# Performance work log

Hardware: AMD Instinct MI355X
Metric: run time of the kernel (lower is better)

## Reference

```python
import jax, jax.numpy as jnp
import numpy as np

V, E, L, T, H, B = 8124, 1024, 24, 512, 16, 2
S = E // H
DFF = E * 8 // 3  # 2730
EPS = 1e-5
SCALE = 1.0 / np.sqrt(E)  # note: 1/sqrt(emb_dim), as in the source


def _pe():
    # sinusoidal positional encoding [T, E]
    pos = jnp.arange(T, dtype=jnp.float32)[:, None]
    div = jnp.exp(jnp.arange(0, E, 2, dtype=jnp.float32) * (-np.log(10000.0) / E))
    pe = jnp.zeros((T, E), jnp.float32)
    pe = pe.at[:, 0::2].set(jnp.sin(pos * div))
    pe = pe.at[:, 1::2].set(jnp.cos(pos * div))
    return pe


def _rms(x, g):
    # NOTE: source takes the mean over the WHOLE tensor (no dim arg)
    rms = jnp.sqrt(jnp.mean(x.astype(jnp.float32) ** 2) + EPS)
    return (x / rms * g).astype(x.dtype)


def setup_inputs() -> dict:
    key = jax.random.key(0)
    ks = jax.random.split(key, 9)
    def w(k, shape):
        return jax.random.normal(k, shape, jnp.float32) * 0.02
    return {
        "tokens": jax.random.randint(ks[0], (B, T), 0, V),
        "emb_table": w(ks[1], (V, E)),
        "Wqkv": w(ks[2], (L, E, 3 * E)), "bqkv": jnp.zeros((L, 3 * E), jnp.float32),
        "Wo": w(ks[3], (L, E, E)), "bo": jnp.zeros((L, E), jnp.float32),
        "W1": w(ks[4], (L, E, DFF)), "b1": jnp.zeros((L, DFF), jnp.float32),
        "W3": w(ks[5], (L, E, DFF)), "b3": jnp.zeros((L, DFF), jnp.float32),
        "W2": w(ks[6], (L, DFF, E)), "b2": jnp.zeros((L, E), jnp.float32),
        "g_mha": jnp.ones((L, E), jnp.float32),
        "g_ff": jnp.ones((L, E), jnp.float32),
        "g_final": jnp.ones((E,), jnp.float32),
        "Wout": w(ks[7], (E, V)), "bout": jnp.zeros((V,), jnp.float32),
    }


def reference(tokens, emb_table, Wqkv, bqkv, Wo, bo, W1, b1, W3, b3, W2, b2,
              g_mha, g_ff, g_final, Wout, bout):
    x = emb_table[tokens] + _pe()[None]  # [B,T,E]
    mask = jnp.tril(jnp.ones((T, T), bool))

    def block(x, p):
        wqkv, bq, wo, bo_, w1, b1_, w3, b3_, w2, b2_, gm, gf = p
        # --- causal MHA ---
        y = _rms(x, gm)
        qkv = (y @ wqkv + bq).reshape(B, T, H, 3, S)
        q = qkv[..., 0, :].transpose(0, 2, 1, 3)  # [B,H,T,S]
        k = qkv[..., 1, :].transpose(0, 2, 1, 3)
        v = qkv[..., 2, :].transpose(0, 2, 1, 3)
        attn = jnp.einsum('bhqd,bhkd->bhqk', q, k).astype(jnp.float32) * SCALE
        attn = jnp.where(mask, attn, -jnp.inf)
        attn = jax.nn.softmax(attn, axis=-1).astype(x.dtype)
        y = jnp.einsum('bhqk,bhkd->bhqd', attn, v)
        y = y.transpose(0, 2, 1, 3).reshape(B, T, E)
        x = x + (y @ wo + bo_)
        # --- SwiGLU FFN ---
        h = _rms(x, gf)
        u = h @ w1 + b1_
        u = u * jax.nn.sigmoid(u) * (h @ w3 + b3_)
        return x + (u @ w2 + b2_), None

    x, _ = jax.lax.scan(block, x, (Wqkv, bqkv, Wo, bo, W1, b1, W3, b3, W2, b2, g_mha, g_ff))
    return _rms(x, g_final) @ Wout + bout  # [B,T,V]
```

## Files before the change

kernel.cpp:

```cpp
#include <hip/hip_runtime.h>
#include <hip/hip_bf16.h>
#include <math.h>

#define EDIM   1024
#define TSEQ   512
#define NBATCH 2
#define NHEAD  16
#define HDIM   64
#define NLAYER 24
#define VOCAB  8124
#define DFFDIM 2730
#define DPAD   2752
#define MTOK   (NBATCH*TSEQ)
#define NELEM  (MTOK*EDIM)
#define EPSF   1e-5f
#define SCALEF (1.0f/32.0f)
#define NEGBIG (-1e30f)

typedef __bf16 bf16x8 __attribute__((ext_vector_type(8)));
typedef __bf16 bf16x4 __attribute__((ext_vector_type(4)));
typedef float  f32x4  __attribute__((ext_vector_type(4)));

#define MFMA(a, b, c) __builtin_amdgcn_mfma_f32_16x16x32_bf16((a), (b), (c), 0, 0, 0)

__device__ __forceinline__ void gl_lds16(const __bf16* g, __bf16* l) {
  __builtin_amdgcn_global_load_lds(
      (const __attribute__((address_space(1))) void*)g,
      (__attribute__((address_space(3))) void*)l, 16, 0, 0);
}
template <int N> __device__ __forceinline__ void vmwait() {
  asm volatile("s_waitcnt vmcnt(%0)" :: "n"(N) : "memory");
}
__device__ __forceinline__ void lgkm_barrier() {
  asm volatile("s_waitcnt lgkmcnt(0)" ::: "memory");
  __builtin_amdgcn_s_barrier();
}

__global__ __launch_bounds__(256) void k_embed(const int* __restrict__ tok,
                                               const float* __restrict__ emb,
                                               float* __restrict__ x) {
  const int bt = blockIdx.x;
  const int t  = bt & (TSEQ - 1);
  const int tk = tok[bt];
  const float* er = emb + (size_t)tk * EDIM;
  float* xr = x + (size_t)bt * EDIM;
  for (int e = threadIdx.x * 4; e < EDIM; e += 256 * 4) {
    float4 v = *(const float4*)(er + e);
    float vv[4] = {v.x, v.y, v.z, v.w};
    float ou[4];
#pragma unroll
    for (int j = 0; j < 4; ++j) {
      int ee = e + j;
      int i2 = ee & ~1;
      float freq = expf(-(float)i2 * (9.210340371976184f / 1024.0f));
      float ang  = (float)t * freq;
      ou[j] = vv[j] + ((ee & 1) ? cosf(ang) : sinf(ang));
    }
    *(float4*)(xr + e) = make_float4(ou[0], ou[1], ou[2], ou[3]);
  }
}

__global__ __launch_bounds__(256) void k_red1f(float* __restrict__ x,
                                               const float* __restrict__ pb,
                                               int np,
                                               const float* __restrict__ bias,
                                               float* __restrict__ part) {
  float s = 0.f;
  const bool fold = (pb != nullptr);
  for (int i = (blockIdx.x * 256 + threadIdx.x) * 4; i < NELEM; i += 256 * 256 * 4) {
    float4 v = *(const float4*)(x + i);
    if (fold) {
      for (int z = 0; z < np; ++z) {
        float4 a = *(const float4*)(pb + (size_t)z * NELEM + i);
        v.x += a.x; v.y += a.y; v.z += a.z; v.w += a.w;
      }
      float4 c = *(const float4*)(bias + (i & (EDIM - 1)));
      v.x += c.x; v.y += c.y; v.z += c.z; v.w += c.w;
      *(float4*)(x + i) = v;
    }
    s += v.x * v.x + v.y * v.y + v.z * v.z + v.w * v.w;
  }
#pragma unroll
  for (int o = 32; o > 0; o >>= 1) s += __shfl_down(s, o);
  __shared__ float sm[4];
  if ((threadIdx.x & 63) == 0) sm[threadIdx.x >> 6] = s;
  __syncthreads();
  if (threadIdx.x == 0) part[blockIdx.x] = sm[0] + sm[1] + sm[2] + sm[3];
}

__device__ __forceinline__ void conv_tile(const float* __restrict__ src,
                                          const float* __restrict__ gk,
                                          __bf16* __restrict__ dst,
                                          int K, int N, int Kpad, int tk, int tn) {
  __shared__ float st[64][65];
  const int k0 = tk << 6, n0 = tn << 6;
  const int tid = threadIdx.x;
  {
    const int r0 = tid >> 4, c4 = (tid & 15) << 2;
#pragma unroll
    for (int i = 0; i < 4; ++i) {
      const int r = r0 + i * 16;
      const int k = k0 + r;
      float4 v = make_float4(0.f, 0.f, 0.f, 0.f);
      if (k < K) {
        const float* sp = src + (size_t)k * N + n0 + c4;
        if (n0 + c4 + 3 < N) v = *(const float4*)sp;
        else {
          if (n0 + c4 + 0 < N) v.x = sp[0];
          if (n0 + c4 + 1 < N) v.y = sp[1];
          if (n0 + c4 + 2 < N) v.z = sp[2];
          if (n0 + c4 + 3 < N) v.w = sp[3];
        }
        if (gk) {
          const float gv = gk[k];
          v.x *= gv; v.y *= gv; v.z *= gv; v.w *= gv;
        }
      }
      st[r][c4 + 0] = v.x; st[r][c4 + 1] = v.y; st[r][c4 + 2] = v.z; st[r][c4 + 3] = v.w;
    }
  }
  __syncthreads();
  {
    const int nl0 = tid >> 3, c8 = (tid & 7) << 3;
#pragma unroll
    for (int i = 0; i < 2; ++i) {
      const int nl = nl0 + i * 32;
      bf16x8 o = {(__bf16)st[c8 + 0][nl], (__bf16)st[c8 + 1][nl],
                  (__bf16)st[c8 + 2][nl], (__bf16)st[c8 + 3][nl],
                  (__bf16)st[c8 + 4][nl], (__bf16)st[c8 + 5][nl],
                  (__bf16)st[c8 + 6][nl], (__bf16)st[c8 + 7][nl]};
      *(bf16x8*)&dst[(size_t)(n0 + nl) * Kpad + k0 + c8] = o;
    }
  }
}

__global__ __launch_bounds__(256) void k_convAll(const float* __restrict__ Wqkv,
                                                 const float* __restrict__ Wo,
                                                 const float* __restrict__ W1,
                                                 const float* __restrict__ W3,
                                                 const float* __restrict__ W2w,
                                                 const float* __restrict__ g_mha,
                                                 const float* __restrict__ g_ff,
                                                 __bf16* qkvT, __bf16* woT,
                                                 __bf16* w1T, __bf16* w3T, __bf16* w2T) {
  int b = blockIdx.x;
  const int l = b / 3088; b -= l * 3088;
  if (b < 768) {
    conv_tile(Wqkv + (size_t)l * 1024 * 3072, g_mha + (size_t)l * EDIM,
              qkvT + (size_t)l * 3072 * 1024, 1024, 3072, 1024, b / 48, b % 48);
  } else if (b < 1024) {
    int t = b - 768;
    conv_tile(Wo + (size_t)l * 1024 * 1024, nullptr,
              woT + (size_t)l * 1024 * 1024, 1024, 1024, 1024, t / 16, t % 16);
  } else if (b < 1712) {
    int t = b - 1024;
    conv_tile(W1 + (size_t)l * 1024 * DFFDIM, g_ff + (size_t)l * EDIM,
              w1T + (size_t)l * DPAD * 1024, 1024, DFFDIM, 1024, t / 43, t % 43);
  } else if (b < 2400) {
    int t = b - 1712;
    conv_tile(W3 + (size_t)l * 1024 * DFFDIM, g_ff + (size_t)l * EDIM,
              w3T + (size_t)l * DPAD * 1024, 1024, DFFDIM, 1024, t / 43, t % 43);
  } else {
    int t = b - 2400;
    conv_tile(W2w + (size_t)l * DFFDIM * 1024, nullptr,
              w2T + (size_t)l * 1024 * DPAD, DFFDIM, 1024, DPAD, t / 16, t % 16);
  }
}

__global__ __launch_bounds__(256) void k_convH(const float* __restrict__ Wout,
                                               const float* __restrict__ g_final,
                                               __bf16* __restrict__ WoutT) {
  conv_tile(Wout, g_final, WoutT, 1024, VOCAB, 1024, blockIdx.x >> 7, blockIdx.x & 127);
}

template <int BN, int MODE, int FUSE>
__global__ __launch_bounds__(256) void mm(
    const __bf16* __restrict__ A, const float* __restrict__ Af,
    const __bf16* __restrict__ B0w, const __bf16* __restrict__ B1w,
    const float* __restrict__ bias0, const float* __restrict__ bias1,
    const float* __restrict__ part,
    float* __restrict__ po, __bf16* __restrict__ ob,
    __bf16* __restrict__ qout, __bf16* __restrict__ kout, __bf16* __restrict__ vout,
    int N, int lda, int ldb, int Ktot) {
  constexpr int DUAL = (MODE == 2) ? 2 : 1;
  constexpr int FN = BN / 32;
  constexpr int BL = (BN == 128) ? 4 : 2 * DUAL;
  __shared__ __bf16 As[2][8][128][8];
  __shared__ __bf16 Bs[2][DUAL][8][BN][8];
  const int tid = threadIdx.x, lane = tid & 63, wave = tid >> 6;
  const int m0 = blockIdx.y << 7, n0 = blockIdx.x * BN;
  const int wm0 = (wave >> 1) * 64, wn0 = (wave & 1) * (BN / 2);
  const int lr = lane & 15, kh = lane >> 4;

  const int ktiles = Ktot >> 6;
  const int nt0 = (ktiles + gridDim.z - 1) / gridDim.z;
  const int tbeg = blockIdx.z * nt0;
  const int tend = (ktiles < tbeg + nt0) ? ktiles : (tbeg + nt0);
  const int nt = tend - tbeg;

  f32x4 acc[DUAL][4][FN];
#pragma unroll
  for (int d = 0; d < DUAL; ++d)
#pragma unroll
    for (int mi = 0; mi < 4; ++mi)
#pragma unroll
      for (int fn = 0; fn < FN; ++fn) acc[d][mi][fn] = (f32x4){0.f, 0.f, 0.f, 0.f};

  float4 ar[4][2];
  auto LOADA = [&](int t) {
    const int k0 = (tbeg + t) << 6;
#pragma unroll
    for (int i = 0; i < 4; ++i) {
      const int d = i * 256 + tid;
      const int row = d >> 3, kb = d & 7;
      const float* ap = Af + (size_t)(m0 + row) * lda + k0 + kb * 8;
      ar[i][0] = *(const float4*)ap; ar[i][1] = *(const float4*)(ap + 4);
    }
  };
  auto DSWA = [&](int buf) {
#pragma unroll
    for (int i = 0; i < 4; ++i) {
      const int d = i * 256 + tid;
      const int row = d >> 3, kb = d & 7;
      float4 a = ar[i][0], b = ar[i][1];
      bf16x8 w = {(__bf16)a.x, (__bf16)a.y, (__bf16)a.z, (__bf16)a.w,
                  (__bf16)b.x, (__bf16)b.y, (__bf16)b.z, (__bf16)b.w};
      *(bf16x8*)&As[buf][kb][row ^ kb][0] = w;
    }
  };
  auto STAGEA_G = [&](int buf, int t) {
    const int k0 = (tbeg + t) << 6;
#pragma unroll
    for (int i = 0; i < 4; ++i) {
      const int d = i * 256 + tid;
      gl_lds16(A + (size_t)(m0 + (d & 127)) * lda + k0 + (d >> 7) * 8,
               &As[buf][d >> 7][d & 127][0]);
    }
  };
  auto STAGEB = [&](int buf, int t) {
    const int k0 = (tbeg + t) << 6;
    if (BN == 128) {
#pragma unroll
      for (int i = 0; i < 4; ++i) {
        const int d = i * 256 + tid;
        gl_lds16(B0w + (size_t)(n0 + (d & 127)) * ldb + k0 + (d >> 7) * 8,
                 &Bs[buf][0][d >> 7][d & 127][0]);
      }
    } else {
#pragma unroll
      for (int i = 0; i < 2; ++i) {
        const int d = i * 256 + tid;
        gl_lds16(B0w + (size_t)(n0 + (d & 63)) * ldb + k0 + (d >> 6) * 8,
                 &Bs[buf][0][d >> 6][d & 63][0]);
      }
      if (DUAL == 2) {
#pragma unroll
        for (int i = 0; i < 2; ++i) {
          const int d = i * 256 + tid;
          gl_lds16(B1w + (size_t)(n0 + (d & 63)) * ldb + k0 + (d >> 6) * 8,
                   &Bs[buf][DUAL - 1][d >> 6][d & 63][0]);
        }
      }
    }
  };
  auto COMP = [&](int buf) {
#pragma unroll
    for (int ks = 0; ks < 2; ++ks) {
      const int kidx = ks * 4 + kh;
      bf16x8 af[4];
#pragma unroll
      for (int mi = 0; mi < 4; ++mi) {
        const int r = wm0 + mi * 16 + lr;
        af[mi] = *(const bf16x8*)&As[buf][kidx][FUSE ? (r ^ kidx) : r][0];
      }
#pragma unroll
      for (int d = 0; d < DUAL; ++d)
#pragma unroll
        for (int fn = 0; fn < FN; ++fn) {
          bf16x8 bfr = *(const bf16x8*)&Bs[buf][d][kidx][wn0 + fn * 16 + lr][0];
#pragma unroll
          for (int mi = 0; mi < 4; ++mi)
            acc[d][mi][fn] = MFMA(af[mi], bfr, acc[d][mi][fn]);
        }
    }
  };

  int cur = 0;
  if (FUSE) {
    LOADA(0); STAGEB(0, 0); DSWA(0);
    asm volatile("s_waitcnt lgkmcnt(0)" ::: "memory");
    vmwait<0>(); __builtin_amdgcn_s_barrier();
    for (int t = 0; t < nt - 1; ++t) {
      LOADA(t + 1);
      STAGEB(cur ^ 1, t + 1);
      COMP(cur);
      DSWA(cur ^ 1);
      asm volatile("s_waitcnt lgkmcnt(0)" ::: "memory");
      vmwait<0>(); __builtin_amdgcn_s_barrier();
      cur ^= 1;
    }
    COMP(cur);
  } else {
    STAGEA_G(0, 0); STAGEB(0, 0);
    for (int t = 0; t < nt - 1; ++t) {
      STAGEA_G(cur ^ 1, t + 1); STAGEB(cur ^ 1, t + 1);
      vmwait<4 + BL>();
      __builtin_amdgcn_s_barrier();
      COMP(cur);
      __builtin_amdgcn_s_barrier();
      cur ^= 1;
    }
    vmwait<0>(); __builtin_amdgcn_s_barrier();
    COMP(cur);
  }

  float sc = 1.0f;
  if (FUSE) {
    __shared__ float smr[4];
    float s = part[tid];
#pragma unroll
    for (int o = 32; o > 0; o >>= 1) s += __shfl_down(s, o);
    if ((tid & 63) == 0) smr[tid >> 6] = s;
    __syncthreads();
    sc = 1.0f / sqrtf((smr[0] + smr[1] + smr[2] + smr[3]) / (float)NELEM + EPSF);
  }

#pragma unroll
  for (int mi = 0; mi < 4; ++mi)
#pragma unroll
    for (int fn = 0; fn < FN; ++fn) {
      const int col = n0 + wn0 + fn * 16 + lr;
      if (MODE == 0) {
        const float bs = bias0[col];
        const int h = col / (3 * HDIM);
        const int rsel = (col >> 6) % 3;
        const int s2 = col & (HDIM - 1);
#pragma unroll
        for (int j = 0; j < 4; ++j) {
          const int row = m0 + wm0 + mi * 16 + (kh << 2) + j;
          const int b = row >> 9, t = row & (TSEQ - 1);
          const float v = acc[0][mi][fn][j] * sc + bs;
          if (rsel == 0)      qout[((size_t)(b * NHEAD + h) * TSEQ + t) * HDIM + s2] = (__bf16)v;
          else if (rsel == 1) kout[((size_t)(b * NHEAD + h) * TSEQ + t) * HDIM + s2] = (__bf16)v;
          else                vout[((size_t)(b * NHEAD + h) * HDIM + s2) * TSEQ + t] = (__bf16)v;
        }
      } else if (MODE == 1) {
        float* pz = po + (size_t)blockIdx.z * NELEM;
#pragma unroll
        for (int j = 0; j < 4; ++j) {
          const int row = m0 + wm0 + mi * 16 + (kh << 2) + j;
          pz[(size_t)row * EDIM + col] = acc[0][mi][fn][j];
        }
      } else if (MODE == 2) {
        const bool ok = col < N;
        const float bb1 = ok ? bias0[col] : 0.f;
        const float bb3 = ok ? bias1[col] : 0.f;
#pragma unroll
        for (int j = 0; j < 4; ++j) {
          const int row = m0 + wm0 + mi * 16 + (kh << 2) + j;
          float v = 0.f;
          if (ok) {
            const float a1v = acc[0][mi][fn][j] * sc + bb1;
            const float a3v = acc[DUAL - 1][mi][fn][j] * sc + bb3;
            v = a1v * (1.0f / (1.0f + __expf(-a1v))) * a3v;
          }
          ob[(size_t)row * DPAD + col] = (__bf16)v;
        }
      } else {
        if (col < N) {
          const float bs = bias0[col];
#pragma unroll
          for (int j = 0; j < 4; ++j) {
            const int row = m0 + wm0 + mi * 16 + (kh << 2) + j;
            po[(size_t)row * N + col] = acc[0][mi][fn][j] * sc + bs;
          }
        }
      }
    }
}

__global__ __launch_bounds__(256) void k_flash(const __bf16* __restrict__ qbuf,
                                               const __bf16* __restrict__ kbuf,
                                               const __bf16* __restrict__ vbufT,
                                               __bf16* __restrict__ y2) {
  const int qt = blockIdx.x, bh = blockIdx.y;
  const int b = bh >> 4, h = bh & 15;
  const int m0 = qt << 5;
  const __bf16* qp = qbuf  + (size_t)bh * TSEQ * HDIM;
  const __bf16* kp = kbuf  + (size_t)bh * TSEQ * HDIM;
  const __bf16* vp = vbufT + (size_t)bh * HDIM * TSEQ;
  __shared__ __bf16 Qs[8][32][8], Ks[2][8][64][8], Vs[2][8][64][8], Ps[8][32][8];
  __shared__ float wmax[2][32], wsum[2][32];
  const int tid = threadIdx.x, lane = tid & 63, wave = tid >> 6;
  const int wm = (wave >> 1) << 4, wn = (wave & 1) << 5;
  const int lr = lane & 15, kh = lane >> 4;

  auto STAGE_KV = [&](int kt2, int buf) {
    const int n0s = kt2 << 6;
#pragma unroll
    for (int i = 0; i < 2; ++i) {
      const int d = i * 256 + tid;
      const int kb2 = d >> 6, row = d & 63;
      gl_lds16(kp + (size_t)(n0s + row) * HDIM + kb2 * 8, &Ks[buf][kb2][row][0]);
      gl_lds16(vp + (size_t)row * TSEQ + n0s + kb2 * 8, &Vs[buf][kb2][row][0]);
    }
  };

  gl_lds16(qp + (size_t)(m0 + (tid & 31)) * HDIM + (tid >> 5) * 8,
           &Qs[tid >> 5][tid & 31][0]);
  STAGE_KV(0, 0);

  float m_[4], l_[4];
#pragma unroll
  for (int j = 0; j < 4; ++j) { m_[j] = NEGBIG; l_[j] = 0.f; }
  f32x4 o0 = {0, 0, 0, 0}, o1 = {0, 0, 0, 0};

  const int ktmax = qt >> 1;
  int cur = 0;
  for (int kt = 0; kt <= ktmax; ++kt) {
    const int n0 = kt << 6;
    if (kt < ktmax) {
      STAGE_KV(kt + 1, cur ^ 1);
      vmwait<4>();
    } else {
      vmwait<0>();
    }
    __builtin_amdgcn_s_barrier();

    f32x4 s0 = {0, 0, 0, 0}, s1 = {0, 0, 0, 0};
#pragma unroll
    for (int ks = 0; ks < 2; ++ks) {
      const int kidx = ks * 4 + kh;
      bf16x8 a  = *(const bf16x8*)&Qs[kidx][wm + lr][0];
      bf16x8 b0 = *(const bf16x8*)&Ks[cur][kidx][wn + lr][0];
      bf16x8 b1 = *(const bf16x8*)&Ks[cur][kidx][wn + 16 + lr][0];
      s0 = MFMA(a, b0, s0); s1 = MFMA(a, b1, s1);
    }
    float pv0[4], pv1[4];
#pragma unroll
    for (int j = 0; j < 4; ++j) {
      const int grow = m0 + wm + (kh << 2) + j;
      float t0 = s0[j] * SCALEF; if (n0 + wn + lr > grow)      t0 = NEGBIG;
      float t1 = s1[j] * SCALEF; if (n0 + wn + 16 + lr > grow) t1 = NEGBIG;
      pv0[j] = t0; pv1[j] = t1;
      float v = fmaxf(t0, t1);
      v = fmaxf(v, __shfl_xor(v, 1)); v = fmaxf(v, __shfl_xor(v, 2));
      v = fmaxf(v, __shfl_xor(v, 4)); v = fmaxf(v, __shfl_xor(v, 8));
      wmax[wave & 1][wm + (kh << 2) + j] = v;
    }
    lgkm_barrier();

    float tmax[4]; bool need = false;
#pragma unroll
    for (int j = 0; j < 4; ++j) {
      const int rl = wm + (kh << 2) + j;
      tmax[j] = fmaxf(wmax[0][rl], wmax[1][rl]);
      need |= (tmax[j] > m_[j] + 8.f);
    }
    if (__ballot(need)) {
#pragma unroll
      for (int j = 0; j < 4; ++j) {
        const float mn = fmaxf(m_[j], tmax[j]);
        const float al = __expf(m_[j] - mn);
        m_[j] = mn; l_[j] *= al; o0[j] *= al; o1[j] *= al;
      }
    }
#pragma unroll
    for (int j = 0; j < 4; ++j) {
      const float p0 = __expf(pv0[j] - m_[j]);
      const float p1 = __expf(pv1[j] - m_[j]);
      float rs = p0 + p1;
      rs += __shfl_xor(rs, 1); rs += __shfl_xor(rs, 2);
      rs += __shfl_xor(rs, 4); rs += __shfl_xor(rs, 8);
      const int rl = wm + (kh << 2) + j;
      wsum[wave & 1][rl] = rs;
      const int pc0 = wn + lr, pc1 = wn + 16 + lr;
      Ps[pc0 >> 3][rl][pc0 & 7] = (__bf16)p0;
      Ps[pc1 >> 3][rl][pc1 & 7] = (__bf16)p1;
    }
    lgkm_barrier();

#pragma unroll
    for (int j = 0; j < 4; ++j) {
      const int rl = wm + (kh << 2) + j;
      l_[j] += wsum[0][rl] + wsum[1][rl];
    }
#pragma unroll
    for (int ks = 0; ks < 2; ++ks) {
      const int kidx = ks * 4 + kh;
      bf16x8 a  = *(const bf16x8*)&Ps[kidx][wm + lr][0];
      bf16x8 b0 = *(const bf16x8*)&Vs[cur][kidx][wn + lr][0];
      bf16x8 b1 = *(const bf16x8*)&Vs[cur][kidx][wn + 16 + lr][0];
      o0 = MFMA(a, b0, o0); o1 = MFMA(a, b1, o1);
    }
    __builtin_amdgcn_s_barrier();
    cur ^= 1;
  }

#pragma unroll
  for (int j = 0; j < 4; ++j) {
    const int row = m0 + wm + (kh << 2) + j;
    const float inv = 1.0f / l_[j];
    y2[((size_t)(b * TSEQ) + row) * EDIM + h * HDIM + wn + lr]      = (__bf16)(o0[j] * inv);
    y2[((size_t)(b * TSEQ) + row) * EDIM + h * HDIM + wn + 16 + lr] = (__bf16)(o1[j] * inv);
  }
}

extern "C" void kernel_launch(void* const* d_in, const int* in_sizes, int n_in,
                              void* d_out, int out_size, void* d_ws, size_t ws_size,
                              hipStream_t stream) {
  const int*   tokens  = (const int*)d_in[0];
  const float* emb     = (const float*)d_in[1];
  const float* Wqkv    = (const float*)d_in[2];
  const float* bqkv    = (const float*)d_in[3];
  const float* Wo      = (const float*)d_in[4];
  const float* bo      = (const float*)d_in[5];
  const float* W1      = (const float*)d_in[6];
  const float* b1      = (const float*)d_in[7];
  const float* W3      = (const float*)d_in[8];
  const float* b3      = (const float*)d_in[9];
  const float* W2w     = (const float*)d_in[10];
  const float* b2      = (const float*)d_in[11];
  const float* g_mha   = (const float*)d_in[12];
  const float* g_ff    = (const float*)d_in[13];
  const float* g_final = (const float*)d_in[14];
  const float* Wout    = (const float*)d_in[15];
  const float* bout    = (const float*)d_in[16];
  float* out = (float*)d_out;

  char* base = (char*)d_ws;
  size_t off = 0;
  auto alloc = [&](size_t bytes) { char* p = base + off; off = (off + bytes + 255) & ~(size_t)255; return p; };
  float*  x    = (float*)alloc(4u << 20);
  float*  part = (float*)alloc(2048);
  __bf16* qbf  = (__bf16*)alloc(2u << 20);
  __bf16* kbf  = (__bf16*)alloc(2u << 20);
  __bf16* vbT  = (__bf16*)alloc(2u << 20);
  __bf16* y2bf = (__bf16*)alloc(2u << 20);
  __bf16* ubf  = (__bf16*)alloc((size_t)MTOK * DPAD * 2);
  float*  pbuf = (float*)alloc((size_t)4 * NELEM * 4);
  __bf16* WoutT = (__bf16*)alloc((size_t)8192 * 1024 * 2);
  __bf16* qkvT = (__bf16*)alloc((size_t)NLAYER * 3072 * 1024 * 2);
  __bf16* woT  = (__bf16*)alloc((size_t)NLAYER * 1024 * 1024 * 2);
  __bf16* w1T  = (__bf16*)alloc((size_t)NLAYER * DPAD * 1024 * 2);
  __bf16* w3T  = (__bf16*)alloc((size_t)NLAYER * DPAD * 1024 * 2);
  __bf16* w2T  = (__bf16*)alloc((size_t)NLAYER * 1024 * DPAD * 2);

  k_embed<<<MTOK, 256, 0, stream>>>(tokens, emb, x);
  k_convAll<<<NLAYER * 3088, 256, 0, stream>>>(Wqkv, Wo, W1, W3, W2w,
                                               g_mha, g_ff,
                                               qkvT, woT, w1T, w3T, w2T);
  k_convH<<<2048, 256, 0, stream>>>(Wout, g_final, WoutT);

  const float* pend_bias = nullptr;
  for (int l = 0; l < NLAYER; ++l) {
    k_red1f<<<256, 256, 0, stream>>>(x, pend_bias ? pbuf : nullptr, 4, pend_bias, part);
    mm<64, 0, 1><<<dim3(48, 8, 1), 256, 0, stream>>>(
        nullptr, x, qkvT + (size_t)l * 3072 * 1024, nullptr,
        bqkv + (size_t)l * 3 * EDIM, nullptr, part,
        nullptr, nullptr, qbf, kbf, vbT, 3072, EDIM, 1024, 1024);
    k_flash<<<dim3(16, 32), 256, 0, stream>>>(qbf, kbf, vbT, y2bf);
    mm<64, 1, 0><<<dim3(16, 8, 4), 256, 0, stream>>>(
        y2bf, nullptr, woT + (size_t)l * 1024 * 1024, nullptr,
        nullptr, nullptr, nullptr,
        pbuf, nullptr, nullptr, nullptr, nullptr, 1024, 1024, 1024, 1024);
    k_red1f<<<256, 256, 0, stream>>>(x, pbuf, 4, bo + (size_t)l * EDIM, part);
    mm<64, 2, 1><<<dim3(43, 8, 1), 256, 0, stream>>>(
        nullptr, x, w1T + (size_t)l * DPAD * 1024, w3T + (size_t)l * DPAD * 1024,
        b1 + (size_t)l * DFFDIM, b3 + (size_t)l * DFFDIM, part,
        nullptr, ubf, nullptr, nullptr, nullptr, DFFDIM, EDIM, 1024, 1024);
    mm<64, 1, 0><<<dim3(16, 8, 4), 256, 0, stream>>>(
        ubf, nullptr, w2T + (size_t)l * 1024 * DPAD, nullptr,
        nullptr, nullptr, nullptr,
        pbuf, nullptr, nullptr, nullptr, nullptr, 1024, DPAD, DPAD, DPAD);
    pend_bias = b2 + (size_t)l * EDIM;
  }

  k_red1f<<<256, 256, 0, stream>>>(x, pbuf, 4, pend_bias, part);
  mm<128, 3, 1><<<dim3(64, 8, 1), 256, 0, stream>>>(
      nullptr, x, WoutT, nullptr, bout, nullptr, part,
      out, nullptr, nullptr, nullptr, nullptr, VOCAB, EDIM, 1024, 1024);
}
```

Baseline: 3.961 ms.

## Emit bf16 activations from reduction kernel and use async LDS loads in GEMMs

The RMS reduction kernel now also writes a bf16 copy of the residual stream. The matmuls read that copy through the async global-to-LDS staging path instead of loading fp32 activations into registers and converting them in-kernel. This removes the register-staged fused A path and halves the A-operand read traffic, at the cost of one extra bf16 write per reduction. Weight conversion also switches to nontemporal loads and stores to avoid polluting the cache.

```diff
diff --git a/kernel.cpp b/kernel.cpp
--- a/kernel.cpp
+++ b/kernel.cpp
@@ -64,7 +64,8 @@
                                                const float* __restrict__ pb,
                                                int np,
                                                const float* __restrict__ bias,
-                                               float* __restrict__ part) {
+                                               float* __restrict__ part,
+                                               __bf16* __restrict__ ybf) {
   float s = 0.f;
   const bool fold = (pb != nullptr);
   for (int i = (blockIdx.x * 256 + threadIdx.x) * 4; i < NELEM; i += 256 * 256 * 4) {
@@ -78,6 +79,8 @@
       v.x += c.x; v.y += c.y; v.z += c.z; v.w += c.w;
       *(float4*)(x + i) = v;
     }
+    bf16x4 o = {(__bf16)v.x, (__bf16)v.y, (__bf16)v.z, (__bf16)v.w};
+    *(bf16x4*)(ybf + i) = o;
     s += v.x * v.x + v.y * v.y + v.z * v.z + v.w * v.w;
   }
 #pragma unroll
@@ -101,22 +104,23 @@
     for (int i = 0; i < 4; ++i) {
       const int r = r0 + i * 16;
       const int k = k0 + r;
-      float4 v = make_float4(0.f, 0.f, 0.f, 0.f);
+      f32x4 v = {0.f, 0.f, 0.f, 0.f};
       if (k < K) {
         const float* sp = src + (size_t)k * N + n0 + c4;
-        if (n0 + c4 + 3 < N) v = *(const float4*)sp;
+        if (n0 + c4 + 3 < N) v = __builtin_nontemporal_load((const f32x4*)sp);
         else {
-          if (n0 + c4 + 0 < N) v.x = sp[0];
-          if (n0 + c4 + 1 < N) v.y = sp[1];
-          if (n0 + c4 + 2 < N) v.z = sp[2];
-          if (n0 + c4 + 3 < N) v.w = sp[3];
+          if (n0 + c4 + 0 < N) v[0] = sp[0];
+          if (n0 + c4 + 1 < N) v[1] = sp[1];
+          if (n0 + c4 + 2 < N) v[2] = sp[2];
+          if (n0 + c4 + 3 < N) v[3] = sp[3];
         }
         if (gk) {
           const float gv = gk[k];
-          v.x *= gv; v.y *= gv; v.z *= gv; v.w *= gv;
-        }
-      }
-      st[r][c4 + 0] = v.x; st[r][c4 + 1] = v.y; st[r][c4 + 2] = v.z; st[r][c4 + 3] = v.w;
+          v[0] *= gv; v[1] *= gv; v[2] *= gv; v[3] *= gv;
+        }
+      }
+      st[r][c4 + 0] = v[0]; st[r][c4 + 1] = v[1];
+      st[r][c4 + 2] = v[2]; st[r][c4 + 3] = v[3];
     }
   }
   __syncthreads();
@@ -129,7 +133,7 @@
                   (__bf16)st[c8 + 2][nl], (__bf16)st[c8 + 3][nl],
                   (__bf16)st[c8 + 4][nl], (__bf16)st[c8 + 5][nl],
                   (__bf16)st[c8 + 6][nl], (__bf16)st[c8 + 7][nl]};
-      *(bf16x8*)&dst[(size_t)(n0 + nl) * Kpad + k0 + c8] = o;
+      __builtin_nontemporal_store(o, (bf16x8*)&dst[(size_t)(n0 + nl) * Kpad + k0 + c8]);
     }
   }
 }
@@ -173,9 +177,9 @@
   conv_tile(Wout, g_final, WoutT, 1024, VOCAB, 1024, blockIdx.x >> 7, blockIdx.x & 127);
 }
 
-template <int BN, int MODE, int FUSE>
+template <int BN, int MODE, int SC>
 __global__ __launch_bounds__(256) void mm(
-    const __bf16* __restrict__ A, const float* __restrict__ Af,
+    const __bf16* __restrict__ A,
     const __bf16* __restrict__ B0w, const __bf16* __restrict__ B1w,
     const float* __restrict__ bias0, const float* __restrict__ bias1,
     const float* __restrict__ part,
@@ -206,29 +210,7 @@
 #pragma unroll
       for (int fn = 0; fn < FN; ++fn) acc[d][mi][fn] = (f32x4){0.f, 0.f, 0.f, 0.f};
 
-  float4 ar[4][2];
-  auto LOADA = [&](int t) {
-    const int k0 = (tbeg + t) << 6;
-#pragma unroll
-    for (int i = 0; i < 4; ++i) {
-      const int d = i * 256 + tid;
-      const int row = d >> 3, kb = d & 7;
-      const float* ap = Af + (size_t)(m0 + row) * lda + k0 + kb * 8;
-      ar[i][0] = *(const float4*)ap; ar[i][1] = *(const float4*)(ap + 4);
-    }
-  };
-  auto DSWA = [&](int buf) {
-#pragma unroll
-    for (int i = 0; i < 4; ++i) {
-      const int d = i * 256 + tid;
-      const int row = d >> 3, kb = d & 7;
-      float4 a = ar[i][0], b = ar[i][1];
-      bf16x8 w = {(__bf16)a.x, (__bf16)a.y, (__bf16)a.z, (__bf16)a.w,
-                  (__bf16)b.x, (__bf16)b.y, (__bf16)b.z, (__bf16)b.w};
-      *(bf16x8*)&As[buf][kb][row ^ kb][0] = w;
-    }
-  };
-  auto STAGEA_G = [&](int buf, int t) {
+  auto STAGE = [&](int buf, int t) {
     const int k0 = (tbeg + t) << 6;
 #pragma unroll
     for (int i = 0; i < 4; ++i) {
@@ -236,9 +218,6 @@
       gl_lds16(A + (size_t)(m0 + (d & 127)) * lda + k0 + (d >> 7) * 8,
                &As[buf][d >> 7][d & 127][0]);
     }
-  };
-  auto STAGEB = [&](int buf, int t) {
-    const int k0 = (tbeg + t) << 6;
     if (BN == 128) {
 #pragma unroll
       for (int i = 0; i < 4; ++i) {
@@ -269,10 +248,8 @@
       const int kidx = ks * 4 + kh;
       bf16x8 af[4];
 #pragma unroll
-      for (int mi = 0; mi < 4; ++mi) {
-        const int r = wm0 + mi * 16 + lr;
-        af[mi] = *(const bf16x8*)&As[buf][kidx][FUSE ? (r ^ kidx) : r][0];
-      }
+      for (int mi = 0; mi < 4; ++mi)
+        af[mi] = *(const bf16x8*)&As[buf][kidx][wm0 + mi * 16 + lr][0];
 #pragma unroll
       for (int d = 0; d < DUAL; ++d)
 #pragma unroll
@@ -285,37 +262,22 @@
     }
   };
 
+  STAGE(0, 0);
   int cur = 0;
-  if (FUSE) {
-    LOADA(0); STAGEB(0, 0); DSWA(0);
-    asm volatile("s_waitcnt lgkmcnt(0)" ::: "memory");
-    vmwait<0>(); __builtin_amdgcn_s_barrier();
-    for (int t = 0; t < nt - 1; ++t) {
-      LOADA(t + 1);
-      STAGEB(cur ^ 1, t + 1);
-      COMP(cur);
-      DSWA(cur ^ 1);
-      asm volatile("s_waitcnt lgkmcnt(0)" ::: "memory");
-      vmwait<0>(); __builtin_amdgcn_s_barrier();
-      cur ^= 1;
-    }
+  for (int t = 0; t < nt - 1; ++t) {
+    STAGE(cur ^ 1, t + 1);
+    vmwait<4 + BL>();
+    __builtin_amdgcn_s_barrier();
     COMP(cur);
-  } else {
-    STAGEA_G(0, 0); STAGEB(0, 0);
-    for (int t = 0; t < nt - 1; ++t) {
-      STAGEA_G(cur ^ 1, t + 1); STAGEB(cur ^ 1, t + 1);
-      vmwait<4 + BL>();
-      __builtin_amdgcn_s_barrier();
-      COMP(cur);
-      __builtin_amdgcn_s_barrier();
-      cur ^= 1;
-    }
-    vmwait<0>(); __builtin_amdgcn_s_barrier();
-    COMP(cur);
-  }
+    __builtin_amdgcn_s_barrier();
+    cur ^= 1;
+  }
+  vmwait<0>();
+  __builtin_amdgcn_s_barrier();
+  COMP(cur);
 
   float sc = 1.0f;
-  if (FUSE) {
+  if (SC) {
     __shared__ float smr[4];
     float s = part[tid];
 #pragma unroll
@@ -533,6 +495,7 @@
   auto alloc = [&](size_t bytes) { char* p = base + off; off = (off + bytes + 255) & ~(size_t)255; return p; };
   float*  x    = (float*)alloc(4u << 20);
   float*  part = (float*)alloc(2048);
+  __bf16* ybf  = (__bf16*)alloc(2u << 20);
   __bf16* qbf  = (__bf16*)alloc(2u << 20);
   __bf16* kbf  = (__bf16*)alloc(2u << 20);
   __bf16* vbT  = (__bf16*)alloc(2u << 20);
@@ -554,30 +517,31 @@
 
   const float* pend_bias = nullptr;
   for (int l = 0; l < NLAYER; ++l) {
-    k_red1f<<<256, 256, 0, stream>>>(x, pend_bias ? pbuf : nullptr, 4, pend_bias, part);
+    k_red1f<<<256, 256, 0, stream>>>(x, pend_bias ? pbuf : nullptr, 4, pend_bias,
+                                     part, ybf);
     mm<64, 0, 1><<<dim3(48, 8, 1), 256, 0, stream>>>(
-        nullptr, x, qkvT + (size_t)l * 3072 * 1024, nullptr,
+        ybf, qkvT + (size_t)l * 3072 * 1024, nullptr,
         bqkv + (size_t)l * 3 * EDIM, nullptr, part,
-        nullptr, nullptr, qbf, kbf, vbT, 3072, EDIM, 1024, 1024);
+        nullptr, nullptr, qbf, kbf, vbT, 3072, 1024, 1024, 1024);
     k_flash<<<dim3(16, 32), 256, 0, stream>>>(qbf, kbf, vbT, y2bf);
     mm<64, 1, 0><<<dim3(16, 8, 4), 256, 0, stream>>>(
-        y2bf, nullptr, woT + (size_t)l * 1024 * 1024, nullptr,
+        y2bf, woT + (size_t)l * 1024 * 1024, nullptr,
         nullptr, nullptr, nullptr,
         pbuf, nullptr, nullptr, nullptr, nullptr, 1024, 1024, 1024, 1024);
-    k_red1f<<<256, 256, 0, stream>>>(x, pbuf, 4, bo + (size_t)l * EDIM, part);
+    k_red1f<<<256, 256, 0, stream>>>(x, pbuf, 4, bo + (size_t)l * EDIM, part, ybf);
     mm<64, 2, 1><<<dim3(43, 8, 1), 256, 0, stream>>>(
-        nullptr, x, w1T + (size_t)l * DPAD * 1024, w3T + (size_t)l * DPAD * 1024,
+        ybf, w1T + (size_t)l * DPAD * 1024, w3T + (size_t)l * DPAD * 1024,
         b1 + (size_t)l * DFFDIM, b3 + (size_t)l * DFFDIM, part,
-        nullptr, ubf, nullptr, nullptr, nullptr, DFFDIM, EDIM, 1024, 1024);
+        nullptr, ubf, nullptr, nullptr, nullptr, DFFDIM, 1024, 1024, 1024);
     mm<64, 1, 0><<<dim3(16, 8, 4), 256, 0, stream>>>(
-        ubf, nullptr, w2T + (size_t)l * 1024 * DPAD, nullptr,
+        ubf, w2T + (size_t)l * 1024 * DPAD, nullptr,
         nullptr, nullptr, nullptr,
         pbuf, nullptr, nullptr, nullptr, nullptr, 1024, DPAD, DPAD, DPAD);
     pend_bias = b2 + (size_t)l * EDIM;
   }
 
-  k_red1f<<<256, 256, 0, stream>>>(x, pbuf, 4, pend_bias, part);
+  k_red1f<<<256, 256, 0, stream>>>(x, pbuf, 4, pend_bias, part, ybf);
   mm<128, 3, 1><<<dim3(64, 8, 1), 256, 0, stream>>>(
-      nullptr, x, WoutT, nullptr, bout, nullptr, part,
-      out, nullptr, nullptr, nullptr, nullptr, VOCAB, EDIM, 1024, 1024);
-}
+      ybf, WoutT, nullptr, bout, nullptr, part,
+      out, nullptr, nullptr, nullptr, nullptr, VOCAB, 1024, 1024, 1024);
+}
```

New measurement: 3.886 ms. Within noise of the previous version (-1.9%).
